# Kernel optimization log

Measured on AMD Instinct MI355X. Metric: run time of the kernel, lower is better.

The kernel has to match this reference:

```python
import jax, jax.numpy as jnp
import numpy as np

B, N, DIM, HEADS, DEPTH = 2, 2048, 1024, 16, 6
HID = 4 * DIM
DH = DIM // HEADS
SCALE = DH ** -0.5
TEMP = 1.0
EPS = 1e-5


def _ln(x, g, b):
    m = jnp.mean(x, axis=-1, keepdims=True)
    v = jnp.var(x, axis=-1, keepdims=True)
    return (x - m) * jax.lax.rsqrt(v + EPS) * g + b


def setup_inputs() -> dict:
    key = jax.random.key(0)
    ks = jax.random.split(key, 10)
    w = lambda k, shape: jax.random.normal(k, shape, dtype=jnp.float32) * 0.02
    return {
        "x": jax.random.normal(ks[0], (B, N, DIM), dtype=jnp.float32),
        "Wqkv": w(ks[1], (DEPTH, DIM, 3 * DIM)),
        "bqkv": jnp.zeros((DEPTH, 3 * DIM), jnp.float32),
        "Wo": w(ks[2], (DEPTH, DIM, DIM)),
        "bo": jnp.zeros((DEPTH, DIM), jnp.float32),
        "W1": w(ks[3], (DEPTH, DIM, HID)),
        "bm1": jnp.zeros((DEPTH, HID), jnp.float32),
        "W2": w(ks[4], (DEPTH, HID, DIM)),
        "bm2": jnp.zeros((DEPTH, DIM), jnp.float32),
        "ln1_g": jnp.ones((DEPTH, DIM), jnp.float32),
        "ln1_b": jnp.zeros((DEPTH, DIM), jnp.float32),
        "ln2_g": jnp.ones((DEPTH, DIM), jnp.float32),
        "ln2_b": jnp.zeros((DEPTH, DIM), jnp.float32),
    }


def reference(x, Wqkv, bqkv, Wo, bo, W1, bm1, W2, bm2, ln1_g, ln1_b, ln2_g, ln2_b):
    def block(xc, p):
        wqkv, bq, wo, bo_, w1, b1_, w2, b2_, g1, be1, g2, be2 = p
        b, n, _ = xc.shape
        # --- PreNorm + Attention ---
        h = _ln(xc, g1, be1)
        qkv = h @ wqkv + bq                       # [b, n, 3*dim]
        q, k, v = jnp.split(qkv, 3, axis=-1)
        split = lambda t: t.reshape(b, n, HEADS, DH).transpose(0, 2, 1, 3)
        q, k, v = split(q), split(k), split(v)    # [b, h, n, d]
        dots = jnp.einsum('bhid,bhjd->bhij', q, k) * SCALE
        attn = jax.nn.softmax(dots, axis=-1) / TEMP
        o = jnp.einsum('bhij,bhjd->bhid', attn, v)
        o = o.transpose(0, 2, 1, 3).reshape(b, n, DIM)
        xc = (o @ wo + bo_) + xc
        # --- PreNorm + MLP (exact GELU, as nn.GELU default) ---
        h2 = _ln(xc, g2, be2)
        m = jax.nn.gelu(h2 @ w1 + b1_, approximate=False) @ w2 + b2_
        return xc + m, None

    params = (Wqkv, bqkv, Wo, bo, W1, bm1, W2, bm2, ln1_g, ln1_b, ln2_g, ln2_b)
    x, _ = jax.lax.scan(block, x, params)
    return x
```

## Files before the change

kernel.cpp:

```cpp
#include <hip/hip_runtime.h>
#include <stdint.h>

#define B_     2
#define N_TOK  2048
#define DIM_   1024
#define HEADS_ 16
#define DEPTH_ 6
#define HID_   4096
#define DH_    64
#define MROWS_ (B_ * N_TOK)
#define SCALE_ 0.125f

typedef __bf16 bf16x8 __attribute__((ext_vector_type(8)));
typedef float  f32x4  __attribute__((ext_vector_type(4)));
typedef float  f32x16 __attribute__((ext_vector_type(16)));

__device__ __forceinline__ unsigned short f2bf(float f) {
  unsigned int u = __float_as_uint(f);
  u += 0x7FFFu + ((u >> 16) & 1u);
  return (unsigned short)(u >> 16);
}

__device__ __forceinline__ f32x4 mfma16(bf16x8 a, bf16x8 b, f32x4 c) {
  return __builtin_amdgcn_mfma_f32_16x16x32_bf16(a, b, c, 0, 0, 0);
}
__device__ __forceinline__ f32x16 mfma32(bf16x8 a, bf16x8 b, f32x16 c) {
  return __builtin_amdgcn_mfma_f32_32x32x16_bf16(a, b, c, 0, 0, 0);
}
__device__ __forceinline__ f32x16 zero16() {
  f32x16 z;
  #pragma unroll
  for (int e = 0; e < 16; ++e) z[e] = 0.f;
  return z;
}

__device__ __forceinline__ void gload_lds16(const unsigned short* g, unsigned short* l) {
  __builtin_amdgcn_global_load_lds(
      (const __attribute__((address_space(1))) unsigned int*)g,
      (__attribute__((address_space(3))) unsigned int*)l, 16, 0, 0);
}

__global__ __launch_bounds__(256) void ln_kernel(
    const float* __restrict__ x, unsigned short* __restrict__ h,
    const float* __restrict__ gw, const float* __restrict__ bw) {
  int row = blockIdx.x;
  int t = threadIdx.x;
  const float* xr = x + (size_t)row * DIM_;
  float4 v = reinterpret_cast<const float4*>(xr)[t];
  float s = v.x + v.y + v.z + v.w;
  float q = v.x * v.x + v.y * v.y + v.z * v.z + v.w * v.w;
  for (int m = 1; m < 64; m <<= 1) { s += __shfl_xor(s, m); q += __shfl_xor(q, m); }
  __shared__ float rs[4], rq[4];
  int lane = t & 63, w = t >> 6;
  if (lane == 0) { rs[w] = s; rq[w] = q; }
  __syncthreads();
  s = rs[0] + rs[1] + rs[2] + rs[3];
  q = rq[0] + rq[1] + rq[2] + rq[3];
  float mean = s * (1.0f / DIM_);
  float var  = q * (1.0f / DIM_) - mean * mean;
  float rstd = rsqrtf(var + 1e-5f);
  float4 gv = reinterpret_cast<const float4*>(gw)[t];
  float4 bv = reinterpret_cast<const float4*>(bw)[t];
  ushort4 ov;
  ov.x = f2bf((v.x - mean) * rstd * gv.x + bv.x);
  ov.y = f2bf((v.y - mean) * rstd * gv.y + bv.y);
  ov.z = f2bf((v.z - mean) * rstd * gv.z + bv.z);
  ov.w = f2bf((v.w - mean) * rstd * gv.w + bv.w);
  reinterpret_cast<ushort4*>(h + (size_t)row * DIM_)[t] = ov;
}

__global__ __launch_bounds__(256) void transpose_w(
    const float* __restrict__ W, unsigned short* __restrict__ Wt, int K, int Nn) {
  __shared__ unsigned short tile[32][33];
  int n0 = blockIdx.x * 32, k0 = blockIdx.y * 32;
  int tx = threadIdx.x & 31, ty = threadIdx.x >> 5;
  #pragma unroll
  for (int r = ty; r < 32; r += 8)
    tile[r][tx] = f2bf(W[(size_t)(k0 + r) * Nn + n0 + tx]);
  __syncthreads();
  #pragma unroll
  for (int r = ty; r < 32; r += 8)
    Wt[(size_t)(n0 + r) * K + k0 + tx] = tile[tx][r];
}

__global__ __launch_bounds__(256) void vtrans(
    const unsigned short* __restrict__ qkv, unsigned short* __restrict__ vt) {
  __shared__ unsigned short t[64][65];
  int b = blockIdx.y >> 4, h = blockIdx.y & 15;
  int n0 = blockIdx.x * 64;
  int tx = threadIdx.x & 63, ty = threadIdx.x >> 6;
  const unsigned short* src = qkv + ((size_t)(b * N_TOK + n0)) * (3 * DIM_) + 2 * DIM_ + h * DH_;
  #pragma unroll
  for (int r = ty; r < 64; r += 4) t[r][tx] = src[(size_t)r * (3 * DIM_) + tx];
  __syncthreads();
  unsigned short* dst = vt + ((size_t)blockIdx.y * DH_) * N_TOK + n0;
  #pragma unroll
  for (int r = ty; r < 64; r += 4) dst[(size_t)r * N_TOK + tx] = t[tx][r];
}

#define EP_BF16       0
#define EP_BF16_GELU  1
#define EP_F32_RESID  2

template <int EP>
__global__ __launch_bounds__(256) void gemm_kernel(
    const unsigned short* __restrict__ A, const unsigned short* __restrict__ Bt,
    const float* __restrict__ bias, unsigned short* __restrict__ Cb,
    float* __restrict__ Cf, int M, int Nn, int K) {
  int brow = blockIdx.x * 128;
  int bcol = blockIdx.y * 128;
  int Ks = K / gridDim.z;
  int kbase = blockIdx.z * Ks;
  int lane = threadIdx.x & 63, wave = threadIdx.x >> 6;
  int i = lane & 15, g = lane >> 4;
  int wr = wave >> 1, wc = wave & 1;
  __shared__ unsigned short Al[2][128 * 32];
  __shared__ unsigned short Bl[2][128 * 32];

  f32x4 zero4 = {0.f, 0.f, 0.f, 0.f};
  f32x4 acc[4][4];
  #pragma unroll
  for (int m = 0; m < 4; ++m)
    #pragma unroll
    for (int n = 0; n < 4; ++n) acc[m][n] = zero4;

  auto stage = [&](int buf, int k0) {
    #pragma unroll
    for (int c = 0; c < 2; ++c) {
      int ch = wave * 2 + c;
      int row = ch * 16 + (lane >> 2);
      int k8 = (lane & 3) * 8;
      gload_lds16(A + (size_t)(brow + row) * K + kbase + k0 + k8, &Al[buf][ch * 512]);
      gload_lds16(Bt + (size_t)(bcol + row) * K + kbase + k0 + k8, &Bl[buf][ch * 512]);
    }
  };

  int NT = Ks / 32;
  stage(0, 0);
  for (int t = 0; t < NT; ++t) {
    __syncthreads();
    if (t + 1 < NT) stage((t + 1) & 1, (t + 1) * 32);
    int buf = t & 1;
    bf16x8 af[4], bfr[4];
    #pragma unroll
    for (int m = 0; m < 4; ++m)
      af[m] = *reinterpret_cast<const bf16x8*>(&Al[buf][(wr * 64 + m * 16 + i) * 32 + g * 8]);
    #pragma unroll
    for (int n = 0; n < 4; ++n)
      bfr[n] = *reinterpret_cast<const bf16x8*>(&Bl[buf][(wc * 64 + n * 16 + i) * 32 + g * 8]);
    #pragma unroll
    for (int m = 0; m < 4; ++m)
      #pragma unroll
      for (int n = 0; n < 4; ++n)
        acc[m][n] = mfma16(af[m], bfr[n], acc[m][n]);
  }

  int rowbase = brow + wr * 64;
  int colbase = bcol + wc * 64;
  #pragma unroll
  for (int m = 0; m < 4; ++m) {
    #pragma unroll
    for (int n = 0; n < 4; ++n) {
      int col = colbase + n * 16 + i;
      float bs = bias[col];
      #pragma unroll
      for (int r = 0; r < 4; ++r) {
        int row = rowbase + m * 16 + g * 4 + r;
        float v = acc[m][n][r] + bs;
        if constexpr (EP == EP_BF16) {
          Cb[(size_t)row * Nn + col] = f2bf(v);
        } else if constexpr (EP == EP_BF16_GELU) {
          float gg = 0.5f * v * (1.0f + erff(v * 0.70710678118f));
          Cb[(size_t)row * Nn + col] = f2bf(gg);
        } else {
          size_t idx = (size_t)row * Nn + col;
          float vv = acc[m][n][r] + (blockIdx.z == 0 ? bs : 0.f);
          atomicAdd(&Cf[idx], vv);
        }
      }
    }
  }
}

__global__ __launch_bounds__(256) void attn_kernel(
    const unsigned short* __restrict__ qkv, const unsigned short* __restrict__ vt,
    unsigned short* __restrict__ o) {
  int qt = blockIdx.x, bh = blockIdx.y;
  int b = bh >> 4, h = bh & 15;
  int tid = threadIdx.x, lane = tid & 63, wave = tid >> 6;
  int q5 = lane & 31, hi = lane >> 5;
  __shared__ unsigned short Kl[2][64 * 64];
  __shared__ unsigned short Vl[2][64 * 64];

  const size_t qstr = 3 * DIM_;
  int qrow = qt * 128 + wave * 32 + q5;

  bf16x8 qa[4];
  #pragma unroll
  for (int f = 0; f < 4; ++f)
    qa[f] = *reinterpret_cast<const bf16x8*>(
        qkv + (size_t)(b * N_TOK + qrow) * qstr + h * DH_ + f * 16 + hi * 8);

  f32x16 oacc[2];
  oacc[0] = zero16(); oacc[1] = zero16();
  float m = -1e30f, l = 0.f;

  const unsigned short* kbase = qkv + (size_t)b * N_TOK * qstr + DIM_ + h * DH_;
  const unsigned short* vbase = vt + (size_t)bh * DH_ * N_TOK;
  uint4 kreg[2], vreg[2];

  auto issue = [&](int j0) {
    #pragma unroll
    for (int p = 0; p < 2; ++p) {
      int c = p * 256 + tid;
      int row = c >> 3, off = c & 7;
      kreg[p] = *reinterpret_cast<const uint4*>(kbase + (size_t)(j0 + row) * qstr + off * 8);
      vreg[p] = *reinterpret_cast<const uint4*>(vbase + (size_t)row * N_TOK + j0 + off * 8);
    }
  };
  auto commit = [&](int buf) {
    #pragma unroll
    for (int p = 0; p < 2; ++p) {
      int c = p * 256 + tid;
      int row = c >> 3, off = c & 7;
      int sw = row * 64 + ((off * 8) ^ ((row & 7) << 3));
      *reinterpret_cast<uint4*>(&Kl[buf][sw]) = kreg[p];
      *reinterpret_cast<uint4*>(&Vl[buf][sw]) = vreg[p];
    }
  };

  issue(0); commit(0);
  int cur = 0;
  for (int jt = 0; jt < N_TOK / 64; ++jt) {
    __syncthreads();
    if (jt + 1 < N_TOK / 64) issue((jt + 1) * 64);

    f32x16 sacc0 = zero16(), sacc1 = zero16();
    #pragma unroll
    for (int f = 0; f < 4; ++f) {
      int r0 = q5;
      int r1 = 32 + q5;
      bf16x8 ka0 = *reinterpret_cast<const bf16x8*>(
          &Kl[cur][r0 * 64 + ((f * 16 + hi * 8) ^ ((r0 & 7) << 3))]);
      bf16x8 ka1 = *reinterpret_cast<const bf16x8*>(
          &Kl[cur][r1 * 64 + ((f * 16 + hi * 8) ^ ((r1 & 7) << 3))]);
      sacc0 = mfma32(ka0, qa[f], sacc0);
      sacc1 = mfma32(ka1, qa[f], sacc1);
    }

    float pe0[16], pe1[16];
    float tmax = -1e30f;
    #pragma unroll
    for (int r = 0; r < 16; ++r) {
      pe0[r] = sacc0[r] * SCALE_;
      pe1[r] = sacc1[r] * SCALE_;
      tmax = fmaxf(tmax, fmaxf(pe0[r], pe1[r]));
    }
    tmax = fmaxf(tmax, __shfl_xor(tmax, 32));
    float mn = fmaxf(m, tmax);
    float al = __expf(m - mn);
    m = mn;
    float ps = 0.f;
    #pragma unroll
    for (int r = 0; r < 16; ++r) {
      pe0[r] = __expf(pe0[r] - mn); ps += pe0[r];
      pe1[r] = __expf(pe1[r] - mn); ps += pe1[r];
    }
    ps += __shfl_xor(ps, 32);
    l = l * al + ps;
    oacc[0] *= al;
    oacc[1] *= al;

    unsigned int cc0[8], cc1[8], dd0[8], dd1[8];
    #pragma unroll
    for (int t = 0; t < 8; ++t) {
      union { __bf16 hh[2]; unsigned int u; } p0, p1;
      p0.hh[0] = (__bf16)pe0[2 * t]; p0.hh[1] = (__bf16)pe0[2 * t + 1];
      p1.hh[0] = (__bf16)pe1[2 * t]; p1.hh[1] = (__bf16)pe1[2 * t + 1];
      cc0[t] = p0.u; cc1[t] = p1.u;
      dd0[t] = __shfl_xor(p0.u, 32);
      dd1[t] = __shfl_xor(p1.u, 32);
    }
    bf16x8 pb[4];
    #pragma unroll
    for (int half = 0; half < 2; ++half) {
      int t0 = half * 4;
      union { unsigned int w[4]; bf16x8 v; } u0, u1;
      u0.w[0] = hi ? dd0[t0 + 2] : cc0[t0 + 0];
      u0.w[1] = hi ? dd0[t0 + 3] : cc0[t0 + 1];
      u0.w[2] = hi ? cc0[t0 + 2] : dd0[t0 + 0];
      u0.w[3] = hi ? cc0[t0 + 3] : dd0[t0 + 1];
      u1.w[0] = hi ? dd1[t0 + 2] : cc1[t0 + 0];
      u1.w[1] = hi ? dd1[t0 + 3] : cc1[t0 + 1];
      u1.w[2] = hi ? cc1[t0 + 2] : dd1[t0 + 0];
      u1.w[3] = hi ? cc1[t0 + 3] : dd1[t0 + 1];
      pb[half] = u0.v;
      pb[2 + half] = u1.v;
    }

    #pragma unroll
    for (int dt = 0; dt < 2; ++dt) {
      int row = dt * 32 + q5;
      #pragma unroll
      for (int ks = 0; ks < 4; ++ks) {
        bf16x8 va = *reinterpret_cast<const bf16x8*>(
            &Vl[cur][row * 64 + ((ks * 16 + hi * 8) ^ ((row & 7) << 3))]);
        oacc[dt] = mfma32(va, pb[ks], oacc[dt]);
      }
    }
    if (jt + 1 < N_TOK / 64) commit(cur ^ 1);
    cur ^= 1;
  }

  float inv = 1.0f / l;
  unsigned short* ob = o + (size_t)(b * N_TOK + qrow) * DIM_ + h * DH_;
  #pragma unroll
  for (int dt = 0; dt < 2; ++dt)
    #pragma unroll
    for (int rq = 0; rq < 4; ++rq) {
      ushort4 st;
      st.x = f2bf(oacc[dt][rq * 4 + 0] * inv);
      st.y = f2bf(oacc[dt][rq * 4 + 1] * inv);
      st.z = f2bf(oacc[dt][rq * 4 + 2] * inv);
      st.w = f2bf(oacc[dt][rq * 4 + 3] * inv);
      *reinterpret_cast<ushort4*>(ob + dt * 32 + rq * 8 + hi * 4) = st;
    }
}

extern "C" void kernel_launch(void* const* d_in, const int* in_sizes, int n_in,
                              void* d_out, int out_size, void* d_ws, size_t ws_size,
                              hipStream_t stream) {
  (void)in_sizes; (void)n_in; (void)out_size; (void)ws_size;
  const float* x_in = (const float*)d_in[0];
  const float* Wqkv = (const float*)d_in[1];
  const float* bqkv = (const float*)d_in[2];
  const float* Wo   = (const float*)d_in[3];
  const float* bo   = (const float*)d_in[4];
  const float* W1   = (const float*)d_in[5];
  const float* bm1  = (const float*)d_in[6];
  const float* W2   = (const float*)d_in[7];
  const float* bm2  = (const float*)d_in[8];
  const float* ln1g = (const float*)d_in[9];
  const float* ln1b = (const float*)d_in[10];
  const float* ln2g = (const float*)d_in[11];
  const float* ln2b = (const float*)d_in[12];
  float* x = (float*)d_out;

  char* ws = (char*)d_ws;
  unsigned short* wt  = (unsigned short*)(ws);
  unsigned short* hbf = (unsigned short*)(ws + (size_t)8  * 1024 * 1024);
  unsigned short* qkv = (unsigned short*)(ws + (size_t)16 * 1024 * 1024);
  unsigned short* vtb = (unsigned short*)(ws + (size_t)40 * 1024 * 1024);
  unsigned short* ob  = (unsigned short*)(ws + (size_t)48 * 1024 * 1024);
  unsigned short* mid = (unsigned short*)(ws + (size_t)56 * 1024 * 1024);

  hipMemcpyAsync(x, x_in, (size_t)MROWS_ * DIM_ * sizeof(float),
                 hipMemcpyDeviceToDevice, stream);

  for (int l = 0; l < DEPTH_; ++l) {
    const float* wqkv_l = Wqkv + (size_t)l * DIM_ * 3 * DIM_;
    const float* wo_l   = Wo   + (size_t)l * DIM_ * DIM_;
    const float* w1_l   = W1   + (size_t)l * DIM_ * HID_;
    const float* w2_l   = W2   + (size_t)l * HID_ * DIM_;

    ln_kernel<<<MROWS_, 256, 0, stream>>>(x, hbf, ln1g + l * DIM_, ln1b + l * DIM_);
    transpose_w<<<dim3(3 * DIM_ / 32, DIM_ / 32), 256, 0, stream>>>(wqkv_l, wt, DIM_, 3 * DIM_);
    gemm_kernel<EP_BF16><<<dim3(MROWS_ / 128, 3 * DIM_ / 128, 1), 256, 0, stream>>>(
        hbf, wt, bqkv + (size_t)l * 3 * DIM_, qkv, nullptr, MROWS_, 3 * DIM_, DIM_);
    vtrans<<<dim3(N_TOK / 64, B_ * HEADS_), 256, 0, stream>>>(qkv, vtb);
    attn_kernel<<<dim3(N_TOK / 128, B_ * HEADS_), 256, 0, stream>>>(qkv, vtb, ob);
    transpose_w<<<dim3(DIM_ / 32, DIM_ / 32), 256, 0, stream>>>(wo_l, wt, DIM_, DIM_);
    gemm_kernel<EP_F32_RESID><<<dim3(MROWS_ / 128, DIM_ / 128, 2), 256, 0, stream>>>(
        ob, wt, bo + (size_t)l * DIM_, nullptr, x, MROWS_, DIM_, DIM_);

    ln_kernel<<<MROWS_, 256, 0, stream>>>(x, hbf, ln2g + l * DIM_, ln2b + l * DIM_);
    transpose_w<<<dim3(HID_ / 32, DIM_ / 32), 256, 0, stream>>>(w1_l, wt, DIM_, HID_);
    gemm_kernel<EP_BF16_GELU><<<dim3(MROWS_ / 128, HID_ / 128, 1), 256, 0, stream>>>(
        hbf, wt, bm1 + (size_t)l * HID_, mid, nullptr, MROWS_, HID_, DIM_);
    transpose_w<<<dim3(DIM_ / 32, HID_ / 32), 256, 0, stream>>>(w2_l, wt, HID_, DIM_);
    gemm_kernel<EP_F32_RESID><<<dim3(MROWS_ / 128, DIM_ / 128, 4), 256, 0, stream>>>(
        mid, wt, bm2 + (size_t)l * DIM_, nullptr, x, MROWS_, DIM_, HID_);
  }
}
```

Measured before the change: 2.332 ms.

## Use 256x256 swizzled GEMM tiles and replace atomic residual with bf16 split-K partials

The GEMM moves to 256x256 block tiles with 512 threads, a K-step of 64 and an XOR-swizzled LDS layout, aiming for more data reuse per block and fewer LDS bank conflicts. The split-K output GEMMs no longer use fp32 atomicAdd into x. Each K-slice writes bf16 partials, which the next LayerNorm kernel (or a final add kernel) sums together with the bias into the residual. This removes atomic traffic and merges the residual add into LN, at the cost of bf16 rounding on the partial sums and larger LDS use per block.

```diff
diff --git a/kernel.cpp b/kernel.cpp
--- a/kernel.cpp
+++ b/kernel.cpp
@@ -10,6 +10,7 @@
 #define DH_    64
 #define MROWS_ (B_ * N_TOK)
 #define SCALE_ 0.125f
+#define PSTR_  ((size_t)MROWS_ * DIM_)
 
 typedef __bf16 bf16x8 __attribute__((ext_vector_type(8)));
 typedef float  f32x4  __attribute__((ext_vector_type(4)));
@@ -20,6 +21,9 @@
   u += 0x7FFFu + ((u >> 16) & 1u);
   return (unsigned short)(u >> 16);
 }
+__device__ __forceinline__ float bf2f(unsigned short u) {
+  return __uint_as_float((unsigned int)u << 16);
+}
 
 __device__ __forceinline__ f32x4 mfma16(bf16x8 a, bf16x8 b, f32x4 c) {
   return __builtin_amdgcn_mfma_f32_16x16x32_bf16(a, b, c, 0, 0, 0);
@@ -40,13 +44,33 @@
       (__attribute__((address_space(3))) unsigned int*)l, 16, 0, 0);
 }
 
-__global__ __launch_bounds__(256) void ln_kernel(
-    const float* __restrict__ x, unsigned short* __restrict__ h,
-    const float* __restrict__ gw, const float* __restrict__ bw) {
+__global__ __launch_bounds__(256) void copy_x(const float4* __restrict__ src,
+                                              float4* __restrict__ dst) {
+  int i = blockIdx.x * 256 + threadIdx.x;
+  dst[i] = src[i];
+}
+
+__global__ __launch_bounds__(256) void ln_fused(
+    float* __restrict__ x, unsigned short* __restrict__ h,
+    const float* __restrict__ gw, const float* __restrict__ bw,
+    const unsigned short* __restrict__ parts, int nparts,
+    const float* __restrict__ bias2) {
   int row = blockIdx.x;
   int t = threadIdx.x;
-  const float* xr = x + (size_t)row * DIM_;
-  float4 v = reinterpret_cast<const float4*>(xr)[t];
+  size_t i4 = (size_t)row * 256 + t;
+  float4* x4 = reinterpret_cast<float4*>(x);
+  float4 v = x4[i4];
+  if (nparts > 0) {
+    float4 bb = reinterpret_cast<const float4*>(bias2)[t];
+    v.x += bb.x; v.y += bb.y; v.z += bb.z; v.w += bb.w;
+    const ushort4* p4 = reinterpret_cast<const ushort4*>(parts);
+    #pragma unroll 4
+    for (int z = 0; z < nparts; ++z) {
+      ushort4 p = p4[(size_t)z * (PSTR_ / 4) + i4];
+      v.x += bf2f(p.x); v.y += bf2f(p.y); v.z += bf2f(p.z); v.w += bf2f(p.w);
+    }
+    x4[i4] = v;
+  }
   float s = v.x + v.y + v.z + v.w;
   float q = v.x * v.x + v.y * v.y + v.z * v.z + v.w * v.w;
   for (int m = 1; m < 64; m <<= 1) { s += __shfl_xor(s, m); q += __shfl_xor(q, m); }
@@ -69,6 +93,23 @@
   reinterpret_cast<ushort4*>(h + (size_t)row * DIM_)[t] = ov;
 }
 
+__global__ __launch_bounds__(256) void final_add(
+    float* __restrict__ x, const unsigned short* __restrict__ parts,
+    const float* __restrict__ bias2) {
+  size_t i4 = (size_t)blockIdx.x * 256 + threadIdx.x;
+  float4* x4 = reinterpret_cast<float4*>(x);
+  float4 v = x4[i4];
+  float4 bb = reinterpret_cast<const float4*>(bias2)[i4 & 255];
+  v.x += bb.x; v.y += bb.y; v.z += bb.z; v.w += bb.w;
+  const ushort4* p4 = reinterpret_cast<const ushort4*>(parts);
+  #pragma unroll
+  for (int z = 0; z < 4; ++z) {
+    ushort4 p = p4[(size_t)z * (PSTR_ / 4) + i4];
+    v.x += bf2f(p.x); v.y += bf2f(p.y); v.z += bf2f(p.z); v.w += bf2f(p.w);
+  }
+  x4[i4] = v;
+}
+
 __global__ __launch_bounds__(256) void transpose_w(
     const float* __restrict__ W, unsigned short* __restrict__ Wt, int K, int Nn) {
   __shared__ unsigned short tile[32][33];
@@ -100,82 +141,89 @@
 
 #define EP_BF16       0
 #define EP_BF16_GELU  1
-#define EP_F32_RESID  2
+#define EP_BF16_PART  3
 
 template <int EP>
-__global__ __launch_bounds__(256) void gemm_kernel(
+__global__ __launch_bounds__(512, 2) void gemm256(
     const unsigned short* __restrict__ A, const unsigned short* __restrict__ Bt,
     const float* __restrict__ bias, unsigned short* __restrict__ Cb,
-    float* __restrict__ Cf, int M, int Nn, int K) {
-  int brow = blockIdx.x * 128;
-  int bcol = blockIdx.y * 128;
+    int M, int Nn, int K) {
+  int brow = blockIdx.x * 256;
+  int bcol = blockIdx.y * 256;
   int Ks = K / gridDim.z;
   int kbase = blockIdx.z * Ks;
-  int lane = threadIdx.x & 63, wave = threadIdx.x >> 6;
+  int tid = threadIdx.x, lane = tid & 63, wave = tid >> 6;
   int i = lane & 15, g = lane >> 4;
-  int wr = wave >> 1, wc = wave & 1;
-  __shared__ unsigned short Al[2][128 * 32];
-  __shared__ unsigned short Bl[2][128 * 32];
+  int wr = wave >> 2, wc = wave & 3;
+  __shared__ unsigned short Al[2][256 * 64];
+  __shared__ unsigned short Bl[2][256 * 64];
 
   f32x4 zero4 = {0.f, 0.f, 0.f, 0.f};
-  f32x4 acc[4][4];
-  #pragma unroll
-  for (int m = 0; m < 4; ++m)
+  f32x4 acc[8][4];
+  #pragma unroll
+  for (int m = 0; m < 8; ++m)
     #pragma unroll
     for (int n = 0; n < 4; ++n) acc[m][n] = zero4;
 
   auto stage = [&](int buf, int k0) {
     #pragma unroll
-    for (int c = 0; c < 2; ++c) {
-      int ch = wave * 2 + c;
-      int row = ch * 16 + (lane >> 2);
-      int k8 = (lane & 3) * 8;
-      gload_lds16(A + (size_t)(brow + row) * K + kbase + k0 + k8, &Al[buf][ch * 512]);
-      gload_lds16(Bt + (size_t)(bcol + row) * K + kbase + k0 + k8, &Bl[buf][ch * 512]);
+    for (int j = 0; j < 4; ++j) {
+      int c = wave * 4 + j;
+      int row = c * 8 + (lane >> 3);
+      int kel = ((lane & 7) ^ (lane >> 3)) << 3;
+      gload_lds16(A + (size_t)(brow + row) * K + kbase + k0 + kel, &Al[buf][c * 512]);
+      gload_lds16(Bt + (size_t)(bcol + row) * K + kbase + k0 + kel, &Bl[buf][c * 512]);
     }
   };
 
-  int NT = Ks / 32;
+  int NT = Ks / 64;
   stage(0, 0);
   for (int t = 0; t < NT; ++t) {
     __syncthreads();
-    if (t + 1 < NT) stage((t + 1) & 1, (t + 1) * 32);
+    if (t + 1 < NT) stage((t + 1) & 1, (t + 1) * 64);
     int buf = t & 1;
-    bf16x8 af[4], bfr[4];
-    #pragma unroll
-    for (int m = 0; m < 4; ++m)
-      af[m] = *reinterpret_cast<const bf16x8*>(&Al[buf][(wr * 64 + m * 16 + i) * 32 + g * 8]);
-    #pragma unroll
-    for (int n = 0; n < 4; ++n)
-      bfr[n] = *reinterpret_cast<const bf16x8*>(&Bl[buf][(wc * 64 + n * 16 + i) * 32 + g * 8]);
-    #pragma unroll
-    for (int m = 0; m < 4; ++m)
+    #pragma unroll
+    for (int kk = 0; kk < 2; ++kk) {
+      bf16x8 af[8], bfr[4];
       #pragma unroll
-      for (int n = 0; n < 4; ++n)
-        acc[m][n] = mfma16(af[m], bfr[n], acc[m][n]);
-  }
-
-  int rowbase = brow + wr * 64;
+      for (int m = 0; m < 8; ++m) {
+        int row = wr * 128 + m * 16 + i;
+        af[m] = *reinterpret_cast<const bf16x8*>(
+            &Al[buf][row * 64 + ((kk * 32 + g * 8) ^ ((i & 7) << 3))]);
+      }
+      #pragma unroll
+      for (int n = 0; n < 4; ++n) {
+        int row = wc * 64 + n * 16 + i;
+        bfr[n] = *reinterpret_cast<const bf16x8*>(
+            &Bl[buf][row * 64 + ((kk * 32 + g * 8) ^ ((i & 7) << 3))]);
+      }
+      #pragma unroll
+      for (int m = 0; m < 8; ++m)
+        #pragma unroll
+        for (int n = 0; n < 4; ++n)
+          acc[m][n] = mfma16(af[m], bfr[n], acc[m][n]);
+    }
+  }
+
+  int rowbase = brow + wr * 128;
   int colbase = bcol + wc * 64;
   #pragma unroll
-  for (int m = 0; m < 4; ++m) {
+  for (int m = 0; m < 8; ++m) {
     #pragma unroll
     for (int n = 0; n < 4; ++n) {
       int col = colbase + n * 16 + i;
-      float bs = bias[col];
       #pragma unroll
       for (int r = 0; r < 4; ++r) {
         int row = rowbase + m * 16 + g * 4 + r;
-        float v = acc[m][n][r] + bs;
         if constexpr (EP == EP_BF16) {
+          float v = acc[m][n][r] + bias[col];
           Cb[(size_t)row * Nn + col] = f2bf(v);
         } else if constexpr (EP == EP_BF16_GELU) {
+          float v = acc[m][n][r] + bias[col];
           float gg = 0.5f * v * (1.0f + erff(v * 0.70710678118f));
           Cb[(size_t)row * Nn + col] = f2bf(gg);
         } else {
-          size_t idx = (size_t)row * Nn + col;
-          float vv = acc[m][n][r] + (blockIdx.z == 0 ? bs : 0.f);
-          atomicAdd(&Cf[idx], vv);
+          Cb[(size_t)blockIdx.z * PSTR_ + (size_t)row * Nn + col] = f2bf(acc[m][n][r]);
         }
       }
     }
@@ -347,15 +395,16 @@
   float* x = (float*)d_out;
 
   char* ws = (char*)d_ws;
-  unsigned short* wt  = (unsigned short*)(ws);
-  unsigned short* hbf = (unsigned short*)(ws + (size_t)8  * 1024 * 1024);
-  unsigned short* qkv = (unsigned short*)(ws + (size_t)16 * 1024 * 1024);
-  unsigned short* vtb = (unsigned short*)(ws + (size_t)40 * 1024 * 1024);
-  unsigned short* ob  = (unsigned short*)(ws + (size_t)48 * 1024 * 1024);
-  unsigned short* mid = (unsigned short*)(ws + (size_t)56 * 1024 * 1024);
-
-  hipMemcpyAsync(x, x_in, (size_t)MROWS_ * DIM_ * sizeof(float),
-                 hipMemcpyDeviceToDevice, stream);
+  const size_t MB = 1024 * 1024;
+  unsigned short* wt   = (unsigned short*)(ws);
+  unsigned short* hbf  = (unsigned short*)(ws + 8  * MB);
+  unsigned short* qkv  = (unsigned short*)(ws + 16 * MB);
+  unsigned short* vtb  = (unsigned short*)(ws + 40 * MB);
+  unsigned short* ob   = (unsigned short*)(ws + 48 * MB);
+  unsigned short* mid  = (unsigned short*)(ws + 56 * MB);
+  unsigned short* parts= (unsigned short*)(ws + 16 * MB);
+
+  copy_x<<<4096, 256, 0, stream>>>((const float4*)x_in, (float4*)x);
 
   for (int l = 0; l < DEPTH_; ++l) {
     const float* wqkv_l = Wqkv + (size_t)l * DIM_ * 3 * DIM_;
@@ -363,22 +412,32 @@
     const float* w1_l   = W1   + (size_t)l * DIM_ * HID_;
     const float* w2_l   = W2   + (size_t)l * HID_ * DIM_;
 
-    ln_kernel<<<MROWS_, 256, 0, stream>>>(x, hbf, ln1g + l * DIM_, ln1b + l * DIM_);
+    ln_fused<<<MROWS_, 256, 0, stream>>>(
+        x, hbf, ln1g + l * DIM_, ln1b + l * DIM_,
+        parts, l == 0 ? 0 : 4, l == 0 ? nullptr : bm2 + (size_t)(l - 1) * DIM_);
+
     transpose_w<<<dim3(3 * DIM_ / 32, DIM_ / 32), 256, 0, stream>>>(wqkv_l, wt, DIM_, 3 * DIM_);
-    gemm_kernel<EP_BF16><<<dim3(MROWS_ / 128, 3 * DIM_ / 128, 1), 256, 0, stream>>>(
-        hbf, wt, bqkv + (size_t)l * 3 * DIM_, qkv, nullptr, MROWS_, 3 * DIM_, DIM_);
+    gemm256<EP_BF16><<<dim3(16, 12, 1), 512, 0, stream>>>(
+        hbf, wt, bqkv + (size_t)l * 3 * DIM_, qkv, MROWS_, 3 * DIM_, DIM_);
+
     vtrans<<<dim3(N_TOK / 64, B_ * HEADS_), 256, 0, stream>>>(qkv, vtb);
     attn_kernel<<<dim3(N_TOK / 128, B_ * HEADS_), 256, 0, stream>>>(qkv, vtb, ob);
+
     transpose_w<<<dim3(DIM_ / 32, DIM_ / 32), 256, 0, stream>>>(wo_l, wt, DIM_, DIM_);
-    gemm_kernel<EP_F32_RESID><<<dim3(MROWS_ / 128, DIM_ / 128, 2), 256, 0, stream>>>(
-        ob, wt, bo + (size_t)l * DIM_, nullptr, x, MROWS_, DIM_, DIM_);
-
-    ln_kernel<<<MROWS_, 256, 0, stream>>>(x, hbf, ln2g + l * DIM_, ln2b + l * DIM_);
+    gemm256<EP_BF16_PART><<<dim3(16, 4, 4), 512, 0, stream>>>(
+        ob, wt, nullptr, parts, MROWS_, DIM_, DIM_);
+
+    ln_fused<<<MROWS_, 256, 0, stream>>>(
+        x, hbf, ln2g + l * DIM_, ln2b + l * DIM_, parts, 4, bo + (size_t)l * DIM_);
+
     transpose_w<<<dim3(HID_ / 32, DIM_ / 32), 256, 0, stream>>>(w1_l, wt, DIM_, HID_);
-    gemm_kernel<EP_BF16_GELU><<<dim3(MROWS_ / 128, HID_ / 128, 1), 256, 0, stream>>>(
-        hbf, wt, bm1 + (size_t)l * HID_, mid, nullptr, MROWS_, HID_, DIM_);
+    gemm256<EP_BF16_GELU><<<dim3(16, 16, 1), 512, 0, stream>>>(
+        hbf, wt, bm1 + (size_t)l * HID_, mid, MROWS_, HID_, DIM_);
+
     transpose_w<<<dim3(DIM_ / 32, HID_ / 32), 256, 0, stream>>>(w2_l, wt, HID_, DIM_);
-    gemm_kernel<EP_F32_RESID><<<dim3(MROWS_ / 128, DIM_ / 128, 4), 256, 0, stream>>>(
-        mid, wt, bm2 + (size_t)l * DIM_, nullptr, x, MROWS_, DIM_, HID_);
-  }
-}
+    gemm256<EP_BF16_PART><<<dim3(16, 4, 4), 512, 0, stream>>>(
+        mid, wt, nullptr, parts, MROWS_, DIM_, HID_);
+  }
+
+  final_add<<<4096, 256, 0, stream>>>(x, parts, bm2 + (size_t)(DEPTH_ - 1) * DIM_);
+}
```

Result: faster. 1.967 ms (-15.7%).
